# Kernel optimization log

Measured on AMD Instinct MI355X. Metric: run time of the kernel, lower is better.

Reference implementation:

```python
import jax, jax.numpy as jnp
import numpy as np

N = 50000
E = 600000
D = 128


def gcn_conv(x, row, col, w, W, b):
    """PyG GCNConv: add self-loops (weight 1), symmetric deg^-1/2 normalization,
    linear transform, edge-weighted scatter-add aggregation, then bias."""
    n = x.shape[0]
    loop = jnp.arange(n)
    r = jnp.concatenate([row, loop])            # source nodes, [E+N]
    c = jnp.concatenate([col, loop])            # target nodes, [E+N]
    ww = jnp.concatenate([w, jnp.ones((n,), x.dtype)])
    deg = jax.ops.segment_sum(ww, c, num_segments=n)          # weighted in-degree
    dinv = jnp.where(deg > 0, jax.lax.rsqrt(deg), jnp.zeros_like(deg))
    norm = dinv[r] * ww * dinv[c]               # [E+N]
    xl = x @ W                                  # [n, D_out]
    msg = norm[:, None] * xl[r]                 # gather + scale, [E+N, D_out]
    out = jax.ops.segment_sum(msg, c, num_segments=n)
    return out + b


def setup_inputs() -> dict:
    key = jax.random.key(0)
    ks = jax.random.split(key, 12)
    x = jax.random.normal(ks[0], (N, D), dtype=jnp.float32)
    edge_index = jax.random.randint(ks[1], (2, E), 0, N, dtype=jnp.int64)
    edge_weights = jax.random.uniform(ks[2], (E,), dtype=jnp.float32)
    s = 1.0 / np.sqrt(D)
    W1 = jax.random.uniform(ks[3], (D, D), jnp.float32, -s, s)
    b1 = jnp.zeros((D,), jnp.float32)
    W2 = jax.random.uniform(ks[4], (D, D), jnp.float32, -s, s)
    b2 = jnp.zeros((D,), jnp.float32)
    W3 = jax.random.uniform(ks[5], (D, D), jnp.float32, -s, s)
    b3 = jnp.zeros((D,), jnp.float32)
    prelu_w = jnp.array(0.25, jnp.float32)
    return {"x": x, "edge_index": edge_index, "edge_weights": edge_weights,
            "W1": W1, "b1": b1, "W2": W2, "b2": b2, "W3": W3, "b3": b3,
            "prelu_w": prelu_w}


def reference(x, edge_index, edge_weights, W1, b1, W2, b2, W3, b3, prelu_w):
    row, col = edge_index[0], edge_index[1]
    # layer 1: GCNConv -> (dropout: eval, identity) -> ELU
    h = gcn_conv(x, row, col, edge_weights, W1, b1)
    h = jax.nn.elu(h)
    # layer 2: GCNConv -> GELU (torch default = exact erf)
    h = gcn_conv(h, row, col, edge_weights, W2, b2)
    h = jax.nn.gelu(h, approximate=False)
    # layer 3: GCNConv -> PReLU (learnable scalar slope)
    h = gcn_conv(h, row, col, edge_weights, W3, b3)
    h = jnp.where(h >= 0, h, prelu_w * h)
    return h
```

## Files before the change

kernel.cpp:

```cpp
#include <hip/hip_runtime.h>
#include <hip/hip_fp16.h>
#include <math.h>

constexpr int D = 128;
constexpr int CAP = 2048;

struct __align__(16) H8 { __half2 h[4]; };

typedef _Float16     half8   __attribute__((ext_vector_type(8)));
typedef float        floatx4 __attribute__((ext_vector_type(4)));
typedef unsigned int uint4v  __attribute__((ext_vector_type(4)));
typedef unsigned int uint2v  __attribute__((ext_vector_type(2)));


__device__ __forceinline__ int detect64(const int* __restrict__ ei) {
  int z = 0;
#pragma unroll
  for (int i = 0; i < 8; ++i) z |= ei[2 * i + 1];
  return (z == 0) ? 1 : 0;
}

__device__ __forceinline__ void load_edge(const int* __restrict__ ei, int e, int nE,
                                          int m64, int n, int& r, int& c) {
  if (m64) { r = ei[2 * (size_t)e]; c = ei[2 * ((size_t)nE + e)]; }
  else     { r = ei[(size_t)e];     c = ei[(size_t)nE + e]; }
  r = min(max(r, 0), n - 1);
  c = min(max(c, 0), n - 1);
}

__global__ void k_setup(const float* __restrict__ W1, const float* __restrict__ W2,
                        const float* __restrict__ W3, __half* __restrict__ Wt,
                        unsigned long long* __restrict__ cntdeg, int n8) {
  int b = blockIdx.x;
  if (b < 24) {
    int m = b >> 3, s = b & 7;
    const float* W = m == 0 ? W1 : (m == 1 ? W2 : W3);
    __half* o = Wt + (size_t)m * D * D;
    int t = threadIdx.x;
    int nn = t & 127;
    int kh = t >> 7;
    int k0 = s * 16 + kh * 8;
    H8 hv;
#pragma unroll
    for (int jj = 0; jj < 4; ++jj) {
      float f0 = W[(size_t)(k0 + 2 * jj)     * D + nn];
      float f1 = W[(size_t)(k0 + 2 * jj + 1) * D + nn];
      hv.h[jj] = __floats2half2_rn(f0, f1);
    }
    *(H8*)(o + (size_t)nn * D + k0) = hv;
  } else {
    int i = (b - 24) * 256 + threadIdx.x;
    if (i < n8) cntdeg[i] = 0ULL;
  }
}

template <int ACT>
__device__ __forceinline__ float act_f(float x) {
  if (ACT == 1) return x > 0.f ? x : expm1f(x);
  if (ACT == 2) return 0.5f * x * (1.0f + erff(x * 0.70710678118654752440f));
  return x;
}

template <int ACT, typename AT>
__device__ __forceinline__ void gemm_body(int bid, const AT* __restrict__ A,
                                          const __half* __restrict__ Wt,
                                          __half* __restrict__ Y, int n) {
  const int wave = threadIdx.x >> 6;
  const int lane = threadIdx.x & 63;
  const int np = lane & 15;
  const int quad = lane >> 4;
  const int node = bid * 64 + wave * 16 + np;
  const int nc = min(node, n - 1);

  half8 b[4];
#pragma unroll
  for (int s = 0; s < 4; ++s) {
    if constexpr (sizeof(AT) == 4) {
      const float* ap = (const float*)A + (size_t)nc * D + s * 32 + quad * 8;
      floatx4 v0 = __builtin_nontemporal_load((const floatx4*)ap);
      floatx4 v1 = __builtin_nontemporal_load((const floatx4*)(ap + 4));
#pragma unroll
      for (int t = 0; t < 4; ++t) {
        b[s][t]     = (_Float16)act_f<ACT>(v0[t]);
        b[s][t + 4] = (_Float16)act_f<ACT>(v1[t]);
      }
    } else {
      half8 raw = __builtin_nontemporal_load(
          (const half8*)((const __half*)A + ((size_t)s * n + nc) * 32 + quad * 8));
#pragma unroll
      for (int t = 0; t < 8; ++t)
        b[s][t] = (_Float16)act_f<ACT>((float)raw[t]);
    }
  }

  floatx4 acc[8];
#pragma unroll
  for (int mt = 0; mt < 8; ++mt) acc[mt] = (floatx4){0.f, 0.f, 0.f, 0.f};

#pragma unroll
  for (int mt = 0; mt < 8; ++mt) {
#pragma unroll
    for (int s = 0; s < 4; ++s) {
      half8 a = *(const half8*)(Wt + (size_t)(mt * 16 + np) * D + s * 32 + quad * 8);
      acc[mt] = __builtin_amdgcn_mfma_f32_16x16x32_f16(a, b[s], acc[mt], 0, 0, 0);
    }
  }

  if (node < n) {
#pragma unroll
    for (int mt = 0; mt < 8; ++mt) {
      __half2 ha = __floats2half2_rn(acc[mt][0], acc[mt][1]);
      __half2 hb = __floats2half2_rn(acc[mt][2], acc[mt][3]);
      uint2v pv;
      pv[0] = *(unsigned int*)&ha;
      pv[1] = *(unsigned int*)&hb;
      int f0 = mt * 16 + quad * 4;
      __builtin_nontemporal_store(
          pv, (uint2v*)(Y + ((size_t)(f0 >> 5) * n + node) * 32 + (f0 & 31)));
    }
  }
}

template <int ACT, typename AT>
__global__ __launch_bounds__(256) void k_gemm(const AT* __restrict__ A,
                                              const __half* __restrict__ Wt,
                                              __half* __restrict__ Y, int n) {
  gemm_body<ACT, AT>(blockIdx.x, A, Wt, Y, n);
}

__global__ __launch_bounds__(256) void k_posgemm(const float* __restrict__ x,
                                                 const __half* __restrict__ Wt,
                                                 __half* __restrict__ Y,
                                                 const int* __restrict__ ei,
                                                 const float* __restrict__ w,
                                                 unsigned long long* __restrict__ cntdeg,
                                                 int2* __restrict__ rc,
                                                 int* __restrict__ pos,
                                                 int nE, int n, int gb) {
  int b = blockIdx.x;
  if (b < gb) {
    gemm_body<0, float>(b, x, Wt, Y, n);
    return;
  }
  int e = (b - gb) * blockDim.x + threadIdx.x;
  if (e >= nE) return;
  int m64 = detect64(ei);
  int r, c;
  load_edge(ei, e, nE, m64, n, r, c);
  rc[e] = make_int2(r, c);
  float wf = fminf(fmaxf(w[e], 0.0f), 65535.0f);
  unsigned long long pk =
      (1ULL << 32) | (unsigned long long)__float2uint_rn(wf * 65536.0f);
  unsigned long long old = atomicAdd(&cntdeg[(size_t)c << 3], pk);
  pos[e] = (int)(old >> 32);
}

__global__ void k_scan1(const unsigned long long* __restrict__ cntdeg,
                        int* __restrict__ offs, int* __restrict__ bsum, int n) {
  __shared__ int s[256];
  int t = threadIdx.x;
  int i = blockIdx.x * 256 + t;
  int v = 0;
  if (i < n) {
    int cn = (int)(cntdeg[(size_t)i << 3] >> 32);
    v = (cn + 3) & ~3;
  }
  s[t] = v;
  __syncthreads();
  for (int off = 1; off < 256; off <<= 1) {
    int x = 0;
    if (t >= off) x = s[t - off];
    __syncthreads();
    if (t >= off) s[t] += x;
    __syncthreads();
  }
  if (i < n) offs[i] = s[t] - v;
  if (t == 255) bsum[blockIdx.x] = s[255];
}

__global__ void k_scan2(const int* __restrict__ bsum, int* __restrict__ boff, int nb) {
  __shared__ int s[256];
  int t = threadIdx.x;
  int v = (t < nb) ? bsum[t] : 0;
  s[t] = v;
  __syncthreads();
  for (int off = 1; off < 256; off <<= 1) {
    int x = 0;
    if (t >= off) x = s[t - off];
    __syncthreads();
    if (t >= off) s[t] += x;
    __syncthreads();
  }
  if (t < nb) boff[t] = s[t] - v;
}

__global__ void k_scan3(int* __restrict__ offs, const int* __restrict__ boff,
                        const int* __restrict__ bsum,
                        const unsigned long long* __restrict__ cntdeg,
                        float* __restrict__ dinv, int n, int nb) {
  int i = blockIdx.x * 256 + threadIdx.x;
  if (i < n) {
    offs[i] += boff[blockIdx.x];
    float degf =
        (float)(unsigned int)(cntdeg[(size_t)i << 3] & 0xffffffffULL) * (1.0f / 65536.0f);
    dinv[i] = rsqrtf(1.0f + degf);
  }
  if (i == 0) offs[n] = boff[nb - 1] + bsum[nb - 1];
}

__global__ void k_fill(const int2* __restrict__ rc, const int* __restrict__ pos,
                       const float* __restrict__ w, const int* __restrict__ offs,
                       const unsigned long long* __restrict__ cntdeg,
                       const float* __restrict__ dinv,
                       unsigned int* __restrict__ ecf2, int nE, int n) {
  int e = blockIdx.x * blockDim.x + threadIdx.x;
  if (e < nE) {
    int2 p = rc[e];
    int idx = offs[p.y] + pos[e];
    float cf = dinv[p.x] * w[e];
    ecf2[idx] = ((unsigned int)p.x << 16) |
                (unsigned int)__half_as_ushort(__float2half_rn(cf));
  }
  if (e < n) {
    int q0 = offs[e] + (int)(cntdeg[(size_t)e << 3] >> 32), q1 = offs[e + 1];
    for (int q = q0; q < q1; ++q) ecf2[q] = 0;
  }
}

__device__ __forceinline__ void fmacc8(float* acc, float c, const H8& y) {
  const _Float16* hp = (const _Float16*)&y;
#pragma unroll
  for (int i = 0; i < 8; ++i) acc[i] = fmaf(c, (float)hp[i], acc[i]);
}

__device__ __forceinline__ float cdecode(unsigned int u) {
  return __half2float(__ushort_as_half((unsigned short)(u & 0xffffu)));
}

__device__ __forceinline__ void gather4(H8* y, uint4v u, const __half* __restrict__ Yc,
                                        int j) {
#pragma unroll
  for (int i = 0; i < 4; ++i)
    y[i] = *(const H8*)(Yc + (size_t)(u[i] >> 16) * 32 + j * 8);
}

__device__ __forceinline__ void accum4(float* acc, uint4v u, const H8* y) {
#pragma unroll
  for (int i = 0; i < 4; ++i) fmacc8(acc, cdecode(u[i]), y[i]);
}

template <int PRELU, typename OutT>
__global__ __launch_bounds__(256) void k_agg(const __half* __restrict__ Y,
                                             const int* __restrict__ offs,
                                             const unsigned int* __restrict__ ecf2,
                                             const float* __restrict__ dinv,
                                             const float* __restrict__ bias,
                                             const float* __restrict__ pw,
                                             OutT* __restrict__ OUT, int n) {
  __shared__ unsigned int sc[CAP];
  const int chunk = blockIdx.x & 3;
  const int t = threadIdx.x;
  const int node0 = (blockIdx.x >> 2) * 32;
  const int node = node0 + (t >> 3);
  const int sub = (t >> 2) & 1;
  const int j = t & 3;

  const int seg_lo = offs[node0];
  const int seg_hi = offs[min(node0 + 32, n)];
  const int segN = min(seg_hi - seg_lo, CAP);
  for (int i = t * 4; i < segN; i += 1024) {
    uint4v v = __builtin_nontemporal_load((const uint4v*)(ecf2 + seg_lo + i));
    *(uint4v*)&sc[i] = v;
  }
  __syncthreads();

  if (node >= n) return;
  const __half* Yc = Y + (size_t)chunk * n * 32;
  float dc = dinv[node];
  float acc[8] = {0.f, 0.f, 0.f, 0.f, 0.f, 0.f, 0.f, 0.f};

  H8 ys{};
  if (sub == 0) ys = *(const H8*)(Yc + (size_t)node * 32 + j * 8);

  int lo = offs[node], hi = offs[node + 1];
  int nb4 = (hi - lo) >> 2;
  int em = lo + (((nb4 + 1) >> 1) << 2);
  int b0 = sub ? em : lo;
  int be = sub ? hi : em;

  for (int b = b0; b < be; b += 8) {
    bool has2 = (be - b) > 4;
    int k0 = b - seg_lo;
    uint4v u0 = (k0 < CAP) ? *(const uint4v*)&sc[k0]
                           : *(const uint4v*)(ecf2 + b);
    uint4v u1{};
    if (has2) {
      int k1 = k0 + 4;
      u1 = (k1 < CAP) ? *(const uint4v*)&sc[k1]
                      : *(const uint4v*)(ecf2 + b + 4);
    }
    H8 y0[4], y1[4];
    gather4(y0, u0, Yc, j);
    if (has2) gather4(y1, u1, Yc, j);
    accum4(acc, u0, y0);
    if (has2) accum4(acc, u1, y1);
  }
  if (sub == 0) fmacc8(acc, dc, ys);

  floatx4 b4 = *(const floatx4*)(bias + chunk * 32 + j * 8 + sub * 4);
  float o[4];
#pragma unroll
  for (int i = 0; i < 4; ++i) {
    float mine  = sub ? acc[4 + i] : acc[i];
    float other = sub ? acc[i]     : acc[4 + i];
    float recv = __shfl_xor(other, 4, 64);
    o[i] = dc * (mine + recv) + b4[i];
  }
  if (PRELU) {
    float wv = *pw;
#pragma unroll
    for (int i = 0; i < 4; ++i) o[i] = o[i] >= 0.f ? o[i] : wv * o[i];
  }
  if constexpr (sizeof(OutT) == 4) {
    floatx4 ov = {o[0], o[1], o[2], o[3]};
    __builtin_nontemporal_store(
        ov, (floatx4*)((float*)OUT + (size_t)node * D + chunk * 32 + j * 8 + sub * 4));
  } else {
    __half2 ha = __floats2half2_rn(o[0], o[1]);
    __half2 hb = __floats2half2_rn(o[2], o[3]);
    uint2v pv;
    pv[0] = *(unsigned int*)&ha;
    pv[1] = *(unsigned int*)&hb;
    __builtin_nontemporal_store(
        pv, (uint2v*)((__half*)OUT + ((size_t)chunk * n + node) * 32 + j * 8 + sub * 4));
  }
}

extern "C" void kernel_launch(void* const* d_in, const int* in_sizes, int n_in,
                              void* d_out, int out_size, void* d_ws, size_t ws_size,
                              hipStream_t stream) {
  const float* x  = (const float*)d_in[0];
  const int*   ei = (const int*)d_in[1];
  const float* w  = (const float*)d_in[2];
  const float* W1 = (const float*)d_in[3];
  const float* b1 = (const float*)d_in[4];
  const float* W2 = (const float*)d_in[5];
  const float* b2 = (const float*)d_in[6];
  const float* W3 = (const float*)d_in[7];
  const float* b3 = (const float*)d_in[8];
  const float* pw = (const float*)d_in[9];
  const int N = in_sizes[0] / D;
  const int E = in_sizes[2];
  float* out = (float*)d_out;

  char* wsb = (char*)d_ws;
  size_t off = 0;
  auto alloc = [&](size_t bytes) {
    void* p = wsb + off;
    off = (off + bytes + 255) & ~(size_t)255;
    return p;
  };
  float*              dinv   = (float*)alloc((size_t)N * 4);
  unsigned long long* cntdeg = (unsigned long long*)alloc((size_t)N * 64);
  int*                offs   = (int*)alloc((size_t)(N + 1) * 4);
  int*                bsum   = (int*)alloc(256 * 4);
  int*                boff   = (int*)alloc(256 * 4);
  unsigned int*       ecf2   = (unsigned int*)alloc(((size_t)E + 3 * (size_t)N + 64) * 4);
  __half*             Wt     = (__half*)alloc((size_t)3 * D * D * 2);
  __half*             Y      = (__half*)alloc((size_t)N * D * 2);
  __half*             h      = (__half*)alloc((size_t)N * D * 2);
  int2*               rc     = (int2*)alloc((size_t)E * 8);
  int*                pos    = (int*)alloc((size_t)E * 4);

  const int nbN = (N + 255) / 256;
  const int eb  = (E + 255) / 256;
  const int fb  = ((E > N ? E : N) + 255) / 256;
  const int n8  = N * 8;
  const int zb  = (n8 + 255) / 256;
  const int gb  = (N + 63) / 64;
  const int ab  = 4 * ((N + 31) / 32);

  hipLaunchKernelGGL(k_setup,   dim3(24 + zb), dim3(256), 0, stream, W1, W2, W3, Wt, cntdeg, n8);
  hipLaunchKernelGGL(k_posgemm, dim3(gb + eb), dim3(256), 0, stream, x, Wt, Y, ei, w, cntdeg,
                     rc, pos, E, N, gb);
  hipLaunchKernelGGL(k_scan1,   dim3(nbN), dim3(256), 0, stream, cntdeg, offs, bsum, N);
  hipLaunchKernelGGL(k_scan2,   dim3(1),   dim3(256), 0, stream, bsum, boff, nbN);
  hipLaunchKernelGGL(k_scan3,   dim3(nbN), dim3(256), 0, stream, offs, boff, bsum, cntdeg, dinv, N, nbN);
  hipLaunchKernelGGL(k_fill,    dim3(fb),  dim3(256), 0, stream, rc, pos, w, offs, cntdeg, dinv, ecf2, E, N);

  hipLaunchKernelGGL((k_agg<0, __half>),  dim3(ab), dim3(256), 0, stream, Y, offs, ecf2, dinv, b1, pw, h, N);
  hipLaunchKernelGGL((k_gemm<1, __half>), dim3(gb), dim3(256), 0, stream, h, Wt + D * D,     Y, N);
  hipLaunchKernelGGL((k_agg<0, __half>),  dim3(ab), dim3(256), 0, stream, Y, offs, ecf2, dinv, b2, pw, h, N);
  hipLaunchKernelGGL((k_gemm<2, __half>), dim3(gb), dim3(256), 0, stream, h, Wt + 2 * D * D, Y, N);
  hipLaunchKernelGGL((k_agg<1, float>),   dim3(ab), dim3(256), 0, stream, Y, offs, ecf2, dinv, b3, pw, out, N);
}
```

Measured before the change: 289.3 us.

## Fuse aggregation with next-layer GEMM and merge scan kernels

Each aggregation block now covers 16 nodes across all 128 features. It applies bias and activation, stages the 16x128 half tile in shared memory, and runs the next layer's MFMA GEMM in the same kernel. This removes the separate GEMM launches and the round trip of the intermediate h through global memory. The scan2 and scan3 kernels are also merged by having every block redo the small block-sum scan. In exchange, each thread does the full edge loop for a node (the previous two-way split is gone), and the coefficient cache is smaller (512 entries), so occupancy and load balance may change.

```diff
diff --git a/kernel.cpp b/kernel.cpp
--- a/kernel.cpp
+++ b/kernel.cpp
@@ -3,7 +3,7 @@
 #include <math.h>
 
 constexpr int D = 128;
-constexpr int CAP = 2048;
+constexpr int CAPF = 512;
 
 struct __align__(16) H8 { __half2 h[4]; };
 
@@ -61,8 +61,7 @@
   return x;
 }
 
-template <int ACT, typename AT>
-__device__ __forceinline__ void gemm_body(int bid, const AT* __restrict__ A,
+__device__ __forceinline__ void gemm_body(int bid, const float* __restrict__ A,
                                           const __half* __restrict__ Wt,
                                           __half* __restrict__ Y, int n) {
   const int wave = threadIdx.x >> 6;
@@ -75,21 +74,13 @@
   half8 b[4];
 #pragma unroll
   for (int s = 0; s < 4; ++s) {
-    if constexpr (sizeof(AT) == 4) {
-      const float* ap = (const float*)A + (size_t)nc * D + s * 32 + quad * 8;
-      floatx4 v0 = __builtin_nontemporal_load((const floatx4*)ap);
-      floatx4 v1 = __builtin_nontemporal_load((const floatx4*)(ap + 4));
-#pragma unroll
-      for (int t = 0; t < 4; ++t) {
-        b[s][t]     = (_Float16)act_f<ACT>(v0[t]);
-        b[s][t + 4] = (_Float16)act_f<ACT>(v1[t]);
-      }
-    } else {
-      half8 raw = __builtin_nontemporal_load(
-          (const half8*)((const __half*)A + ((size_t)s * n + nc) * 32 + quad * 8));
-#pragma unroll
-      for (int t = 0; t < 8; ++t)
-        b[s][t] = (_Float16)act_f<ACT>((float)raw[t]);
+    const float* ap = A + (size_t)nc * D + s * 32 + quad * 8;
+    floatx4 v0 = __builtin_nontemporal_load((const floatx4*)ap);
+    floatx4 v1 = __builtin_nontemporal_load((const floatx4*)(ap + 4));
+#pragma unroll
+    for (int t = 0; t < 4; ++t) {
+      b[s][t]     = (_Float16)v0[t];
+      b[s][t + 4] = (_Float16)v1[t];
     }
   }
 
@@ -119,13 +110,6 @@
           pv, (uint2v*)(Y + ((size_t)(f0 >> 5) * n + node) * 32 + (f0 & 31)));
     }
   }
-}
-
-template <int ACT, typename AT>
-__global__ __launch_bounds__(256) void k_gemm(const AT* __restrict__ A,
-                                              const __half* __restrict__ Wt,
-                                              __half* __restrict__ Y, int n) {
-  gemm_body<ACT, AT>(blockIdx.x, A, Wt, Y, n);
 }
 
 __global__ __launch_bounds__(256) void k_posgemm(const float* __restrict__ x,
@@ -139,7 +123,7 @@
                                                  int nE, int n, int gb) {
   int b = blockIdx.x;
   if (b < gb) {
-    gemm_body<0, float>(b, x, Wt, Y, n);
+    gemm_body(b, x, Wt, Y, n);
     return;
   }
   int e = (b - gb) * blockDim.x + threadIdx.x;
@@ -178,7 +162,9 @@
   if (t == 255) bsum[blockIdx.x] = s[255];
 }
 
-__global__ void k_scan2(const int* __restrict__ bsum, int* __restrict__ boff, int nb) {
+__global__ void k_scan23(int* __restrict__ offs, const int* __restrict__ bsum,
+                         const unsigned long long* __restrict__ cntdeg,
+                         float* __restrict__ dinv, int n, int nb) {
   __shared__ int s[256];
   int t = threadIdx.x;
   int v = (t < nb) ? bsum[t] : 0;
@@ -191,21 +177,16 @@
     if (t >= off) s[t] += x;
     __syncthreads();
   }
-  if (t < nb) boff[t] = s[t] - v;
-}
-
-__global__ void k_scan3(int* __restrict__ offs, const int* __restrict__ boff,
-                        const int* __restrict__ bsum,
-                        const unsigned long long* __restrict__ cntdeg,
-                        float* __restrict__ dinv, int n, int nb) {
-  int i = blockIdx.x * 256 + threadIdx.x;
+  int b = blockIdx.x;
+  int boffb = (b == 0) ? 0 : s[b - 1];
+  int i = b * 256 + t;
   if (i < n) {
-    offs[i] += boff[blockIdx.x];
+    offs[i] += boffb;
     float degf =
         (float)(unsigned int)(cntdeg[(size_t)i << 3] & 0xffffffffULL) * (1.0f / 65536.0f);
     dinv[i] = rsqrtf(1.0f + degf);
   }
-  if (i == 0) offs[n] = boff[nb - 1] + bsum[nb - 1];
+  if (i == 0) offs[n] = s[nb - 1];
 }
 
 __global__ void k_fill(const int2* __restrict__ rc, const int* __restrict__ pos,
@@ -249,90 +230,135 @@
   for (int i = 0; i < 4; ++i) fmacc8(acc, cdecode(u[i]), y[i]);
 }
 
-template <int PRELU, typename OutT>
-__global__ __launch_bounds__(256) void k_agg(const __half* __restrict__ Y,
-                                             const int* __restrict__ offs,
-                                             const unsigned int* __restrict__ ecf2,
-                                             const float* __restrict__ dinv,
-                                             const float* __restrict__ bias,
-                                             const float* __restrict__ pw,
-                                             OutT* __restrict__ OUT, int n) {
-  __shared__ unsigned int sc[CAP];
-  const int chunk = blockIdx.x & 3;
-  const int t = threadIdx.x;
-  const int node0 = (blockIdx.x >> 2) * 32;
-  const int node = node0 + (t >> 3);
-  const int sub = (t >> 2) & 1;
-  const int j = t & 3;
-
-  const int seg_lo = offs[node0];
-  const int seg_hi = offs[min(node0 + 32, n)];
-  const int segN = min(seg_hi - seg_lo, CAP);
-  for (int i = t * 4; i < segN; i += 1024) {
-    uint4v v = __builtin_nontemporal_load((const uint4v*)(ecf2 + seg_lo + i));
-    *(uint4v*)&sc[i] = v;
-  }
+#define AGG_PHASE()                                                              \
+  const int nl = t >> 4;                                                         \
+  const int node = node0 + nl;                                                   \
+  const int cj = t & 15;                                                         \
+  const int chunk = cj >> 2, j = cj & 3;                                         \
+  const __half* Yc = Yin + (size_t)chunk * n * 32;                               \
+  const int ncl = min(node, n - 1);                                              \
+  float dc = dinv[ncl];                                                          \
+  float acc[8] = {0.f, 0.f, 0.f, 0.f, 0.f, 0.f, 0.f, 0.f};                       \
+  H8 ys = *(const H8*)(Yc + (size_t)ncl * 32 + j * 8);                           \
+  {                                                                              \
+    int lo = soff[nl], hi = soff[nl + 1];                                        \
+    for (int b = lo; b < hi; b += 8) {                                           \
+      bool has2 = (hi - b) > 4;                                                  \
+      int k0 = b - seg_lo;                                                       \
+      uint4v u0 = (k0 + 4 <= CAPF) ? *(const uint4v*)&sc[k0]                     \
+                                   : *(const uint4v*)(ecf2 + b);                 \
+      uint4v u1{};                                                               \
+      if (has2) {                                                                \
+        int k1 = k0 + 4;                                                         \
+        u1 = (k1 + 4 <= CAPF) ? *(const uint4v*)&sc[k1]                          \
+                              : *(const uint4v*)(ecf2 + b + 4);                  \
+      }                                                                          \
+      H8 y0[4], y1[4];                                                           \
+      gather4(y0, u0, Yc, j);                                                    \
+      if (has2) gather4(y1, u1, Yc, j);                                          \
+      accum4(acc, u0, y0);                                                       \
+      if (has2) accum4(acc, u1, y1);                                             \
+    }                                                                            \
+    fmacc8(acc, dc, ys);                                                         \
+  }
+
+#define STAGE_COEFS()                                                            \
+  const int t = threadIdx.x;                                                     \
+  const int node0 = blockIdx.x * 16;                                             \
+  if (node0 >= n) return;                                                        \
+  const int seg_lo = offs[node0];                                                \
+  const int seg_hi = offs[min(node0 + 16, n)];                                   \
+  const int segN = min(seg_hi - seg_lo, CAPF);                                   \
+  for (int i = t * 4; i < segN; i += 1024)                                       \
+    *(uint4v*)&sc[i] =                                                           \
+        __builtin_nontemporal_load((const uint4v*)(ecf2 + seg_lo + i));          \
+  if (t < 17) soff[t] = offs[min(node0 + t, n)];                                 \
   __syncthreads();
 
-  if (node >= n) return;
-  const __half* Yc = Y + (size_t)chunk * n * 32;
-  float dc = dinv[node];
-  float acc[8] = {0.f, 0.f, 0.f, 0.f, 0.f, 0.f, 0.f, 0.f};
-
-  H8 ys{};
-  if (sub == 0) ys = *(const H8*)(Yc + (size_t)node * 32 + j * 8);
-
-  int lo = offs[node], hi = offs[node + 1];
-  int nb4 = (hi - lo) >> 2;
-  int em = lo + (((nb4 + 1) >> 1) << 2);
-  int b0 = sub ? em : lo;
-  int be = sub ? hi : em;
-
-  for (int b = b0; b < be; b += 8) {
-    bool has2 = (be - b) > 4;
-    int k0 = b - seg_lo;
-    uint4v u0 = (k0 < CAP) ? *(const uint4v*)&sc[k0]
-                           : *(const uint4v*)(ecf2 + b);
-    uint4v u1{};
-    if (has2) {
-      int k1 = k0 + 4;
-      u1 = (k1 < CAP) ? *(const uint4v*)&sc[k1]
-                      : *(const uint4v*)(ecf2 + b + 4);
-    }
-    H8 y0[4], y1[4];
-    gather4(y0, u0, Yc, j);
-    if (has2) gather4(y1, u1, Yc, j);
-    accum4(acc, u0, y0);
-    if (has2) accum4(acc, u1, y1);
-  }
-  if (sub == 0) fmacc8(acc, dc, ys);
-
-  floatx4 b4 = *(const floatx4*)(bias + chunk * 32 + j * 8 + sub * 4);
-  float o[4];
-#pragma unroll
-  for (int i = 0; i < 4; ++i) {
-    float mine  = sub ? acc[4 + i] : acc[i];
-    float other = sub ? acc[i]     : acc[4 + i];
-    float recv = __shfl_xor(other, 4, 64);
-    o[i] = dc * (mine + recv) + b4[i];
-  }
-  if (PRELU) {
+template <int ACT>
+__global__ __launch_bounds__(256, 6) void k_aggemm(
+    const __half* __restrict__ Yin, const int* __restrict__ offs,
+    const unsigned int* __restrict__ ecf2, const float* __restrict__ dinv,
+    const float* __restrict__ bias, const __half* __restrict__ Wt,
+    __half* __restrict__ Yout, int n) {
+  __shared__ unsigned int sc[CAPF];
+  __shared__ __half ht[16 * 136];
+  __shared__ int soff[17];
+  STAGE_COEFS();
+  {
+    AGG_PHASE();
+    floatx4 ba = *(const floatx4*)(bias + chunk * 32 + j * 8);
+    floatx4 bb = *(const floatx4*)(bias + chunk * 32 + j * 8 + 4);
+    float o[8];
+#pragma unroll
+    for (int i = 0; i < 8; ++i)
+      o[i] = act_f<ACT>(dc * acc[i] + (i < 4 ? ba[i] : bb[i - 4]));
+    H8 hw;
+#pragma unroll
+    for (int i = 0; i < 4; ++i) hw.h[i] = __floats2half2_rn(o[2 * i], o[2 * i + 1]);
+    if (node < n) *(H8*)&ht[nl * 136 + chunk * 32 + j * 8] = hw;
+  }
+  __syncthreads();
+
+  const int wave = t >> 6, lane = t & 63, np = lane & 15, quad = lane >> 4;
+  half8 bfr[4];
+#pragma unroll
+  for (int s = 0; s < 4; ++s)
+    bfr[s] = *(const half8*)&ht[np * 136 + s * 32 + quad * 8];
+  floatx4 ga0 = (floatx4){0.f, 0.f, 0.f, 0.f};
+  floatx4 ga1 = (floatx4){0.f, 0.f, 0.f, 0.f};
+#pragma unroll
+  for (int s = 0; s < 4; ++s) {
+    half8 a0 = *(const half8*)(Wt + (size_t)((wave * 2) * 16 + np) * D + s * 32 + quad * 8);
+    ga0 = __builtin_amdgcn_mfma_f32_16x16x32_f16(a0, bfr[s], ga0, 0, 0, 0);
+    half8 a1 = *(const half8*)(Wt + (size_t)((wave * 2 + 1) * 16 + np) * D + s * 32 + quad * 8);
+    ga1 = __builtin_amdgcn_mfma_f32_16x16x32_f16(a1, bfr[s], ga1, 0, 0, 0);
+  }
+  const int gnode = node0 + np;
+  if (gnode < n) {
+    floatx4 g[2] = {ga0, ga1};
+#pragma unroll
+    for (int mi = 0; mi < 2; ++mi) {
+      int mt = wave * 2 + mi;
+      __half2 ha = __floats2half2_rn(g[mi][0], g[mi][1]);
+      __half2 hb = __floats2half2_rn(g[mi][2], g[mi][3]);
+      uint2v pv;
+      pv[0] = *(unsigned int*)&ha;
+      pv[1] = *(unsigned int*)&hb;
+      int f0 = mt * 16 + quad * 4;
+      __builtin_nontemporal_store(
+          pv, (uint2v*)(Yout + ((size_t)(f0 >> 5) * n + gnode) * 32 + (f0 & 31)));
+    }
+  }
+}
+
+__global__ __launch_bounds__(256, 6) void k_aggout(
+    const __half* __restrict__ Yin, const int* __restrict__ offs,
+    const unsigned int* __restrict__ ecf2, const float* __restrict__ dinv,
+    const float* __restrict__ bias, const float* __restrict__ pw,
+    float* __restrict__ out, int n) {
+  __shared__ unsigned int sc[CAPF];
+  __shared__ int soff[17];
+  STAGE_COEFS();
+  AGG_PHASE();
+  if (node < n) {
+    floatx4 ba = *(const floatx4*)(bias + chunk * 32 + j * 8);
+    floatx4 bb = *(const floatx4*)(bias + chunk * 32 + j * 8 + 4);
     float wv = *pw;
-#pragma unroll
-    for (int i = 0; i < 4; ++i) o[i] = o[i] >= 0.f ? o[i] : wv * o[i];
-  }
-  if constexpr (sizeof(OutT) == 4) {
-    floatx4 ov = {o[0], o[1], o[2], o[3]};
-    __builtin_nontemporal_store(
-        ov, (floatx4*)((float*)OUT + (size_t)node * D + chunk * 32 + j * 8 + sub * 4));
-  } else {
-    __half2 ha = __floats2half2_rn(o[0], o[1]);
-    __half2 hb = __floats2half2_rn(o[2], o[3]);
-    uint2v pv;
-    pv[0] = *(unsigned int*)&ha;
-    pv[1] = *(unsigned int*)&hb;
-    __builtin_nontemporal_store(
-        pv, (uint2v*)((__half*)OUT + ((size_t)chunk * n + node) * 32 + j * 8 + sub * 4));
+    floatx4 v0, v1;
+#pragma unroll
+    for (int i = 0; i < 4; ++i) {
+      float o = dc * acc[i] + ba[i];
+      v0[i] = o >= 0.f ? o : wv * o;
+    }
+#pragma unroll
+    for (int i = 0; i < 4; ++i) {
+      float o = dc * acc[4 + i] + bb[i];
+      v1[i] = o >= 0.f ? o : wv * o;
+    }
+    float* op = out + (size_t)node * D + chunk * 32 + j * 8;
+    __builtin_nontemporal_store(v0, (floatx4*)op);
+    __builtin_nontemporal_store(v1, (floatx4*)(op + 4));
   }
 }
 
@@ -364,11 +390,10 @@
   unsigned long long* cntdeg = (unsigned long long*)alloc((size_t)N * 64);
   int*                offs   = (int*)alloc((size_t)(N + 1) * 4);
   int*                bsum   = (int*)alloc(256 * 4);
-  int*                boff   = (int*)alloc(256 * 4);
   unsigned int*       ecf2   = (unsigned int*)alloc(((size_t)E + 3 * (size_t)N + 64) * 4);
   __half*             Wt     = (__half*)alloc((size_t)3 * D * D * 2);
-  __half*             Y      = (__half*)alloc((size_t)N * D * 2);
-  __half*             h      = (__half*)alloc((size_t)N * D * 2);
+  __half*             Ya     = (__half*)alloc((size_t)N * D * 2);
+  __half*             Yb     = (__half*)alloc((size_t)N * D * 2);
   int2*               rc     = (int2*)alloc((size_t)E * 8);
   int*                pos    = (int*)alloc((size_t)E * 4);
 
@@ -378,19 +403,16 @@
   const int n8  = N * 8;
   const int zb  = (n8 + 255) / 256;
   const int gb  = (N + 63) / 64;
-  const int ab  = 4 * ((N + 31) / 32);
+  const int abf = (N + 15) / 16;
 
   hipLaunchKernelGGL(k_setup,   dim3(24 + zb), dim3(256), 0, stream, W1, W2, W3, Wt, cntdeg, n8);
-  hipLaunchKernelGGL(k_posgemm, dim3(gb + eb), dim3(256), 0, stream, x, Wt, Y, ei, w, cntdeg,
+  hipLaunchKernelGGL(k_posgemm, dim3(gb + eb), dim3(256), 0, stream, x, Wt, Ya, ei, w, cntdeg,
                      rc, pos, E, N, gb);
   hipLaunchKernelGGL(k_scan1,   dim3(nbN), dim3(256), 0, stream, cntdeg, offs, bsum, N);
-  hipLaunchKernelGGL(k_scan2,   dim3(1),   dim3(256), 0, stream, bsum, boff, nbN);
-  hipLaunchKernelGGL(k_scan3,   dim3(nbN), dim3(256), 0, stream, offs, boff, bsum, cntdeg, dinv, N, nbN);
+  hipLaunchKernelGGL(k_scan23,  dim3(nbN), dim3(256), 0, stream, offs, bsum, cntdeg, dinv, N, nbN);
   hipLaunchKernelGGL(k_fill,    dim3(fb),  dim3(256), 0, stream, rc, pos, w, offs, cntdeg, dinv, ecf2, E, N);
 
-  hipLaunchKernelGGL((k_agg<0, __half>),  dim3(ab), dim3(256), 0, stream, Y, offs, ecf2, dinv, b1, pw, h, N);
-  hipLaunchKernelGGL((k_gemm<1, __half>), dim3(gb), dim3(256), 0, stream, h, Wt + D * D,     Y, N);
-  hipLaunchKernelGGL((k_agg<0, __half>),  dim3(ab), dim3(256), 0, stream, Y, offs, ecf2, dinv, b2, pw, h, N);
-  hipLaunchKernelGGL((k_gemm<2, __half>), dim3(gb), dim3(256), 0, stream, h, Wt + 2 * D * D, Y, N);
-  hipLaunchKernelGGL((k_agg<1, float>),   dim3(ab), dim3(256), 0, stream, Y, offs, ecf2, dinv, b3, pw, out, N);
-}
+  hipLaunchKernelGGL((k_aggemm<1>), dim3(abf), dim3(256), 0, stream, Ya, offs, ecf2, dinv, b1, Wt + D * D,     Yb, N);
+  hipLaunchKernelGGL((k_aggemm<2>), dim3(abf), dim3(256), 0, stream, Yb, offs, ecf2, dinv, b2, Wt + 2 * D * D, Ya, N);
+  hipLaunchKernelGGL(k_aggout,      dim3(abf), dim3(256), 0, stream, Ya, offs, ecf2, dinv, b3, pw, out, N);
+}
```

Result: no change. 289.4 us (+0.0%).
